# Kernel optimization log

Hardware: AMD Instinct MI355X
Metric: run time of the kernel (lower is better)

Reference implementation:

```python
import jax, jax.numpy as jnp
import numpy as np

N, E, H = 50000, 300000, 8  # nodes, edges, FeaStConv heads (PyG default)


def _lin_init(k, fan_in, fan_out):
    k1, k2 = jax.random.split(k)
    s = 1.0 / np.sqrt(fan_in)
    w = jax.random.uniform(k1, (fan_in, fan_out), jnp.float32, -s, s)
    b = jax.random.uniform(k2, (fan_out,), jnp.float32, -s, s)
    return w, b


def _conv_init(k, cin, cout):
    k1, k2 = jax.random.split(k)
    w = jax.random.normal(k1, (cin, H * cout), jnp.float32) * 0.1   # weight
    u = jax.random.normal(k2, (cin, H), jnp.float32) * 0.1          # attention u
    c = jnp.zeros((H,), jnp.float32)                                 # attention bias
    b = jnp.zeros((cout,), jnp.float32)                              # output bias
    return w, u, c, b


def setup_inputs() -> dict:
    key = jax.random.key(0)
    ks = jax.random.split(key, 10)
    x = jax.random.normal(ks[0], (N, 3), jnp.float32)
    src = jax.random.randint(ks[1], (E,), 0, N)
    dst = jax.random.randint(ks[2], (E,), 0, N)
    dst = jnp.where(src == dst, (dst + 1) % N, dst)  # no self loops in raw edge list
    edge_index = jnp.stack([src, dst]).astype(jnp.int64)
    labels = (jax.random.uniform(ks[3], (N, 1)) < 0.1).astype(jnp.float32)
    lin1_w, lin1_b = _lin_init(ks[4], 3, 16)
    c1_w, c1_u, c1_c, c1_b = _conv_init(ks[5], 16, 32)
    c2_w, c2_u, c2_c, c2_b = _conv_init(ks[6], 32, 64)
    c3_w, c3_u, c3_c, c3_b = _conv_init(ks[7], 64, 128)
    lin2_w, lin2_b = _lin_init(ks[8], 128, 1024)
    lin3_w, lin3_b = _lin_init(ks[9], 1024, 1)
    return dict(x=x, edge_index=edge_index, labels=labels,
                lin1_w=lin1_w, lin1_b=lin1_b,
                c1_w=c1_w, c1_u=c1_u, c1_c=c1_c, c1_b=c1_b,
                c2_w=c2_w, c2_u=c2_u, c2_c=c2_c, c2_b=c2_b,
                c3_w=c3_w, c3_u=c3_u, c3_c=c3_c, c3_b=c3_b,
                lin2_w=lin2_w, lin2_b=lin2_b, lin3_w=lin3_w, lin3_b=lin3_b)


def feast_conv(x, src, dst, W, u, c, b):
    """PyG FeaStConv: gather x_i/x_j, head-softmax attention on (x_j - x_i),
    per-edge weighted sum over heads, mean-scatter to destination nodes."""
    n = x.shape[0]
    loop = jnp.arange(n, dtype=src.dtype)
    s = jnp.concatenate([src, loop])  # add self loops (PyG default)
    d = jnp.concatenate([dst, loop])
    xi = x[d]
    xj = x[s]
    q = jax.nn.softmax((xj - xi) @ u + c, axis=-1)           # [E+N, H]
    m = (xj @ W).reshape(xj.shape[0], H, -1)                  # [E+N, H, O]
    msg = jnp.einsum('eh,eho->eo', q, m)                      # [E+N, O]
    agg = jax.ops.segment_sum(msg, d, num_segments=n)
    cnt = jax.ops.segment_sum(jnp.ones_like(d, dtype=msg.dtype), d, num_segments=n)
    return agg / cnt[:, None] + b                             # mean aggregation + bias


def reference(x, edge_index, labels,
              lin1_w, lin1_b,
              c1_w, c1_u, c1_c, c1_b,
              c2_w, c2_u, c2_c, c2_b,
              c3_w, c3_u, c3_c, c3_b,
              lin2_w, lin2_b, lin3_w, lin3_b):
    src, dst = edge_index[0], edge_index[1]
    h = jax.nn.relu(x @ lin1_w + lin1_b)
    h = jax.nn.relu(feast_conv(h, src, dst, c1_w, c1_u, c1_c, c1_b))
    h = jax.nn.relu(feast_conv(h, src, dst, c2_w, c2_u, c2_c, c2_b))
    h = jax.nn.relu(feast_conv(h, src, dst, c3_w, c3_u, c3_c, c3_b))
    h = jax.nn.relu(h @ lin2_w + lin2_b)
    p = jax.nn.sigmoid(h @ lin3_w + lin3_b)                   # [N, 1]
    # generate_weights: class-balanced per-element BCE weights
    n = labels.shape[0]
    pos = jnp.sum(labels)
    neg = n - pos
    w = jnp.where(labels == 1, n / (2.0 * pos), n / (2.0 * neg))
    # torch-style BCE with log clamped at -100
    bce = -(labels * jnp.clip(jnp.log(p), -100.0, None)
            + (1.0 - labels) * jnp.clip(jnp.log(1.0 - p), -100.0, None))
    loss = jnp.mean(w * bce)
    return loss, p
```

## Files before the change

### kernel.cpp

```cpp
#include <hip/hip_runtime.h>
#include <math.h>

#define NN 50000
#define NE 300000

typedef short s8v __attribute__((ext_vector_type(8)));
typedef float f4v __attribute__((ext_vector_type(4)));

__device__ inline unsigned short f2bf(float f) {
    union { float f; unsigned int u; } v; v.f = f;
    unsigned int r = v.u + 0x7FFFu + ((v.u >> 16) & 1u);
    return (unsigned short)(r >> 16);
}

__global__ void lin1_kernel(const float* __restrict__ x,
                            const float* __restrict__ w,
                            const float* __restrict__ b,
                            float* __restrict__ out) {
    int idx = blockIdx.x * 256 + threadIdx.x;
    if (idx >= NN * 16) return;
    int n = idx >> 4, o = idx & 15;
    float v = x[n*3+0]*w[o] + x[n*3+1]*w[16+o] + x[n*3+2]*w[32+o] + b[o];
    out[idx] = fmaxf(v, 0.f);
}

template<int CIN>
__global__ void a_kernel(const float* __restrict__ h,
                         const float* __restrict__ u,
                         float* __restrict__ a) {
    int idx = blockIdx.x * 256 + threadIdx.x;
    if (idx >= NN * 8) return;
    int n = idx >> 3, hd = idx & 7;
    float acc = 0.f;
    #pragma unroll
    for (int k = 0; k < CIN; ++k) acc += h[(size_t)n*CIN + k] * u[k*8 + hd];
    a[idx] = acc;
}

__global__ void hist_kernel(const int* __restrict__ dst, int* __restrict__ cnt) {
    int e = blockIdx.x * 256 + threadIdx.x;
    if (e < NE) atomicAdd(&cnt[dst[e]], 1);
}

__global__ void scan1_kernel(const int* __restrict__ cnt, int* __restrict__ rp,
                             int* __restrict__ bpart) {
    __shared__ int sh[256];
    int tid = threadIdx.x;
    int gid = blockIdx.x * 256 + tid;
    int v = (gid < NN) ? cnt[gid] : 0;
    sh[tid] = v;
    __syncthreads();
    for (int off = 1; off < 256; off <<= 1) {
        int t = (tid >= off) ? sh[tid - off] : 0;
        __syncthreads();
        sh[tid] += t;
        __syncthreads();
    }
    if (gid < NN) rp[gid] = sh[tid] - v;
    if (tid == 255) bpart[blockIdx.x] = sh[tid];
}

__global__ void scan2_kernel(int* __restrict__ bpart, int nblk) {
    __shared__ int sh[256];
    int tid = threadIdx.x;
    int v = (tid < nblk) ? bpart[tid] : 0;
    sh[tid] = v;
    __syncthreads();
    for (int off = 1; off < 256; off <<= 1) {
        int t = (tid >= off) ? sh[tid - off] : 0;
        __syncthreads();
        sh[tid] += t;
        __syncthreads();
    }
    bpart[tid] = sh[tid] - v;
}

__global__ void scan3_kernel(int* __restrict__ rp, const int* __restrict__ bpart) {
    int gid = blockIdx.x * 256 + threadIdx.x;
    if (gid < NN) rp[gid] += bpart[blockIdx.x];
    if (gid == 0) rp[NN] = NE;
}

__global__ void scatter_kernel(const int* __restrict__ src, const int* __restrict__ dst,
                               const int* __restrict__ rp, int* __restrict__ fill,
                               int* __restrict__ ssrc, int* __restrict__ sdst) {
    int e = blockIdx.x * 256 + threadIdx.x;
    if (e >= NE) return;
    int d = dst[e];
    int pos = rp[d] + atomicAdd(&fill[d], 1);
    ssrc[pos] = src[e];
    sdst[pos] = d;
}

__global__ void q_sorted_kernel(const int* __restrict__ ssrc,
                                const int* __restrict__ sdst,
                                const float* __restrict__ a,
                                const float* __restrict__ c,
                                float* __restrict__ qs) {
    int j = blockIdx.x * 256 + threadIdx.x;
    if (j >= NE) return;
    int s = ssrc[j], d = sdst[j];
    const float4* as = (const float4*)(a + (size_t)s*8);
    const float4* ad = (const float4*)(a + (size_t)d*8);
    float4 s0 = as[0], s1 = as[1], d0 = ad[0], d1 = ad[1];
    float lg[8] = { s0.x-d0.x+c[0], s0.y-d0.y+c[1], s0.z-d0.z+c[2], s0.w-d0.w+c[3],
                    s1.x-d1.x+c[4], s1.y-d1.y+c[5], s1.z-d1.z+c[6], s1.w-d1.w+c[7] };
    float m = lg[0];
    #pragma unroll
    for (int h = 1; h < 8; ++h) m = fmaxf(m, lg[h]);
    float sum = 0.f;
    #pragma unroll
    for (int h = 0; h < 8; ++h) { lg[h] = __expf(lg[h]-m); sum += lg[h]; }
    float inv = 1.f / sum;
    float4* qp = (float4*)(qs + (size_t)j*8);
    qp[0] = make_float4(lg[0]*inv, lg[1]*inv, lg[2]*inv, lg[3]*inv);
    qp[1] = make_float4(lg[4]*inv, lg[5]*inv, lg[6]*inv, lg[7]*inv);
}

template<int HPER>
__device__ inline void load_qv(const float* __restrict__ qs, int j, int hg, float* qv) {
    if constexpr (HPER == 2) {
        float2 t = *(const float2*)(qs + (size_t)j*8 + hg*2);
        qv[0] = t.x; qv[1] = t.y;
    } else if constexpr (HPER == 4) {
        float4 t = *(const float4*)(qs + (size_t)j*8 + hg*4);
        qv[0] = t.x; qv[1] = t.y; qv[2] = t.z; qv[3] = t.w;
    } else {
        float4 t0 = *(const float4*)(qs + (size_t)j*8);
        float4 t1 = *(const float4*)(qs + (size_t)j*8 + 4);
        qv[0] = t0.x; qv[1] = t0.y; qv[2] = t0.z; qv[3] = t0.w;
        qv[4] = t1.x; qv[5] = t1.y; qv[6] = t1.z; qv[7] = t1.w;
    }
}

template<int CIN>
__global__ __launch_bounds__(256) void agg_kernel(
        const float* __restrict__ hin, const float* __restrict__ cbias,
        const int* __restrict__ rowptr, const int* __restrict__ ssrc,
        const float* __restrict__ qs, unsigned short* __restrict__ g) {
    constexpr int HPER = CIN / 8;
    constexpr int LG = (CIN == 16) ? 4 : (CIN == 32) ? 5 : 6;
    const int lane = threadIdx.x & 63;
    const int d = blockIdx.x * 4 + (threadIdx.x >> 6);
    const int k = lane & (CIN - 1);
    const int hg = lane >> LG;
    float m = cbias[0];
    #pragma unroll
    for (int h = 1; h < 8; ++h) m = fmaxf(m, cbias[h]);
    float ssum = 0.f;
    #pragma unroll
    for (int h = 0; h < 8; ++h) ssum += __expf(cbias[h] - m);
    float sinv = 1.f / ssum;
    float xd = hin[(size_t)d*CIN + k];
    float acc[HPER];
    #pragma unroll
    for (int i = 0; i < HPER; ++i)
        acc[i] = __expf(cbias[hg*HPER + i] - m) * sinv * xd;
    int j0 = rowptr[d], j1 = rowptr[d+1];
    int j = j0;
    for (; j + 2 <= j1; j += 2) {
        int s0 = ssrc[j], s1 = ssrc[j+1];
        float xv0 = hin[(size_t)s0*CIN + k];
        float xv1 = hin[(size_t)s1*CIN + k];
        float qv0[HPER], qv1[HPER];
        load_qv<HPER>(qs, j, hg, qv0);
        load_qv<HPER>(qs, j+1, hg, qv1);
        #pragma unroll
        for (int i = 0; i < HPER; ++i) acc[i] += qv0[i]*xv0 + qv1[i]*xv1;
    }
    if (j < j1) {
        int s0 = ssrc[j];
        float xv0 = hin[(size_t)s0*CIN + k];
        float qv0[HPER];
        load_qv<HPER>(qs, j, hg, qv0);
        #pragma unroll
        for (int i = 0; i < HPER; ++i) acc[i] += qv0[i]*xv0;
    }
    #pragma unroll
    for (int i = 0; i < HPER; ++i)
        g[(size_t)d*(8*CIN) + (hg*HPER + i)*CIN + k] = f2bf(acc[i]);
}

template<int CIN, int O>
__global__ void packw_feast(const float* __restrict__ W, unsigned short* __restrict__ wp) {
    constexpr int NS = (8*CIN) / 32;
    constexpr int TOT = (O/16) * NS * 64;
    int t = blockIdx.x * 256 + threadIdx.x;
    if (t >= TOT) return;
    int l = t & 63;
    int s = (t >> 6) % NS;
    int ct = t / (64 * NS);
    int c = ct*16 + (l & 15);
    int kk0 = s*32 + (l >> 4) * 8;
    union { unsigned short u[8]; s8v v; } o;
    #pragma unroll
    for (int i = 0; i < 8; ++i) {
        int kk = kk0 + i;
        int h = kk / CIN, k = kk & (CIN - 1);
        o.u[i] = f2bf(W[(size_t)k*(8*O) + h*O + c]);
    }
    *(s8v*)(wp + (size_t)t*8) = o.v;
}

__global__ void packw_lin(const float* __restrict__ W, unsigned short* __restrict__ wp) {
    int t = blockIdx.x * 256 + threadIdx.x;
    if (t >= 64*4*64) return;
    int l = t & 63;
    int s = (t >> 6) & 3;
    int ctg = t >> 8;
    int c = ctg*16 + (l & 15);
    int k0 = s*32 + (l >> 4) * 8;
    union { unsigned short u[8]; s8v v; } o;
    #pragma unroll
    for (int i = 0; i < 8; ++i) o.u[i] = f2bf(W[(size_t)(k0+i)*1024 + c]);
    *(s8v*)(wp + (size_t)t*8) = o.v;
}

template<int K, int O, int CH, bool BF16OUT>
__global__ __launch_bounds__(256) void gemm_feast(
        const unsigned short* __restrict__ g, const unsigned short* __restrict__ wp,
        const int* __restrict__ rowptr, const float* __restrict__ b,
        float* __restrict__ houtf, unsigned short* __restrict__ houtb) {
    constexpr int NS = K / 32;
    constexpr int NCT = O / 16;
    __shared__ unsigned short bsh[CH*NS*64*8];
    const int l = threadIdx.x & 63;
    const int w = threadIdx.x >> 6;
    const int base = blockIdx.x * 64 + w * 16;
    int arow = base + (l & 15); if (arow >= NN) arow = NN - 1;
    const int koff = (l >> 4) * 8;
    s8v af[NS];
    #pragma unroll
    for (int s = 0; s < NS; ++s)
        af[s] = *(const s8v*)(g + (size_t)arow*K + s*32 + koff);
    float invc[4];
    #pragma unroll
    for (int r = 0; r < 4; ++r) {
        int n = base + (l >> 4)*4 + r; if (n >= NN) n = NN - 1;
        invc[r] = 1.f / (float)(rowptr[n+1] - rowptr[n] + 1);
    }
    #pragma unroll 1
    for (int ct0 = 0; ct0 < NCT; ct0 += CH) {
        __syncthreads();
        const int4* sp = (const int4*)(wp + (size_t)ct0*NS*512);
        int4* dp = (int4*)bsh;
        #pragma unroll 1
        for (int i = threadIdx.x; i < CH*NS*64; i += 256) dp[i] = sp[i];
        __syncthreads();
        #pragma unroll 1
        for (int cc = 0; cc < CH; ++cc) {
            f4v acc = {0.f, 0.f, 0.f, 0.f};
            #pragma unroll
            for (int s = 0; s < NS; ++s) {
                s8v bf = *(const s8v*)(bsh + ((size_t)(cc*NS + s)*64 + l)*8);
                acc = __builtin_amdgcn_mfma_f32_16x16x32_bf16(af[s], bf, acc, 0, 0, 0);
            }
            int col = (ct0 + cc)*16 + (l & 15);
            float bb = b[col];
            #pragma unroll
            for (int r = 0; r < 4; ++r) {
                int n = base + (l >> 4)*4 + r;
                float v = fmaxf(acc[r]*invc[r] + bb, 0.f);
                if (n < NN) {
                    if constexpr (BF16OUT) houtb[(size_t)n*O + col] = f2bf(v);
                    else                   houtf[(size_t)n*O + col] = v;
                }
            }
        }
    }
}

__global__ __launch_bounds__(256) void lin23_mfma(
        const unsigned short* __restrict__ h4b, const unsigned short* __restrict__ w2p,
        const float* __restrict__ b2, const float* __restrict__ w3,
        const float* __restrict__ b3, float* __restrict__ p) {
    constexpr int CH = 8;
    __shared__ unsigned short bsh[CH*4*64*8];
    const int l = threadIdx.x & 63;
    const int w = threadIdx.x >> 6;
    const int base = blockIdx.x * 64 + w * 16;
    int arow = base + (l & 15); if (arow >= NN) arow = NN - 1;
    const int koff = (l >> 4) * 8;
    s8v af[4];
    #pragma unroll
    for (int s = 0; s < 4; ++s)
        af[s] = *(const s8v*)(h4b + (size_t)arow*128 + s*32 + koff);
    float zp0 = 0.f, zp1 = 0.f, zp2 = 0.f, zp3 = 0.f;
    #pragma unroll 1
    for (int ct0 = 0; ct0 < 64; ct0 += CH) {
        __syncthreads();
        const int4* sp = (const int4*)(w2p + (size_t)ct0*4*512);
        int4* dp = (int4*)bsh;
        #pragma unroll 1
        for (int i = threadIdx.x; i < CH*4*64; i += 256) dp[i] = sp[i];
        __syncthreads();
        #pragma unroll 1
        for (int cc = 0; cc < CH; ++cc) {
            f4v acc = {0.f, 0.f, 0.f, 0.f};
            #pragma unroll
            for (int s = 0; s < 4; ++s) {
                s8v bf = *(const s8v*)(bsh + ((size_t)(cc*4 + s)*64 + l)*8);
                acc = __builtin_amdgcn_mfma_f32_16x16x32_bf16(af[s], bf, acc, 0, 0, 0);
            }
            int col = (ct0 + cc)*16 + (l & 15);
            float w3c = w3[col], bb = b2[col];
            zp0 += fmaxf(acc[0] + bb, 0.f) * w3c;
            zp1 += fmaxf(acc[1] + bb, 0.f) * w3c;
            zp2 += fmaxf(acc[2] + bb, 0.f) * w3c;
            zp3 += fmaxf(acc[3] + bb, 0.f) * w3c;
        }
    }
    #pragma unroll
    for (int off = 1; off < 16; off <<= 1) {
        zp0 += __shfl_xor(zp0, off, 64);
        zp1 += __shfl_xor(zp1, off, 64);
        zp2 += __shfl_xor(zp2, off, 64);
        zp3 += __shfl_xor(zp3, off, 64);
    }
    if ((l & 15) == 0) {
        int r0 = base + (l >> 4) * 4;
        float bb3 = b3[0];
        if (r0+0 < NN) p[r0+0] = 1.f / (1.f + expf(-(zp0 + bb3)));
        if (r0+1 < NN) p[r0+1] = 1.f / (1.f + expf(-(zp1 + bb3)));
        if (r0+2 < NN) p[r0+2] = 1.f / (1.f + expf(-(zp2 + bb3)));
        if (r0+3 < NN) p[r0+3] = 1.f / (1.f + expf(-(zp3 + bb3)));
    }
}

__global__ void loss_pass_kernel(const float* __restrict__ labels,
                                 const float* __restrict__ p,
                                 float* __restrict__ scal) {
    __shared__ float sh0[256], sh1[256], sh2[256];
    int tid = threadIdx.x;
    float pos = 0.f, sp = 0.f, sn = 0.f;
    for (int n = blockIdx.x*256 + tid; n < NN; n += gridDim.x*256) {
        float yv = labels[n], pv = p[n];
        if (yv == 1.0f) { pos += 1.f; sp -= fmaxf(logf(pv), -100.f); }
        else            { sn -= fmaxf(logf(1.f - pv), -100.f); }
    }
    sh0[tid] = pos; sh1[tid] = sp; sh2[tid] = sn;
    __syncthreads();
    for (int off = 128; off; off >>= 1) {
        if (tid < off) {
            sh0[tid] += sh0[tid+off];
            sh1[tid] += sh1[tid+off];
            sh2[tid] += sh2[tid+off];
        }
        __syncthreads();
    }
    if (tid == 0) {
        atomicAdd(&scal[0], sh0[0]);
        atomicAdd(&scal[1], sh1[0]);
        atomicAdd(&scal[2], sh2[0]);
    }
}

__global__ void loss_final_kernel(const float* __restrict__ scal,
                                  float* __restrict__ out) {
    float pos = scal[0];
    out[0] = scal[1] / (2.f*pos) + scal[2] / (2.f*((float)NN - pos));
}

extern "C" void kernel_launch(void* const* d_in, const int* in_sizes, int n_in,
                              void* d_out, int out_size, void* d_ws, size_t ws_size,
                              hipStream_t stream) {
    (void)in_sizes; (void)n_in; (void)out_size; (void)ws_size;
    const float* x   = (const float*)d_in[0];
    const int*   ei  = (const int*)d_in[1];
    const float* labels = (const float*)d_in[2];
    const float* l1w = (const float*)d_in[3];
    const float* l1b = (const float*)d_in[4];
    const float* cw[3] = {(const float*)d_in[5], (const float*)d_in[9],  (const float*)d_in[13]};
    const float* cu[3] = {(const float*)d_in[6], (const float*)d_in[10], (const float*)d_in[14]};
    const float* cc[3] = {(const float*)d_in[7], (const float*)d_in[11], (const float*)d_in[15]};
    const float* cb[3] = {(const float*)d_in[8], (const float*)d_in[12], (const float*)d_in[16]};
    const float* l2w = (const float*)d_in[17];
    const float* l2b = (const float*)d_in[18];
    const float* l3w = (const float*)d_in[19];
    const float* l3b = (const float*)d_in[20];
    const int* srcp = ei;
    const int* dstp = ei + NE;
    float* out = (float*)d_out;

    float* ws = (float*)d_ws;
    size_t off = 0;
    auto alloc = [&](size_t n) { float* p = ws + off; off += (n + 15) & ~(size_t)15; return p; };
    float* hA = alloc((size_t)NN*64);
    float* hB = alloc((size_t)NN*128);
    float* a  = alloc((size_t)NN*8);
    unsigned short* g  = (unsigned short*)alloc((size_t)NN*256);
    unsigned short* w2p = (unsigned short*)alloc(65536);
    unsigned short* wfp = (unsigned short*)alloc(32768);
    float* scal = alloc(16);
    int* rowptr = (int*)alloc(50016);
    int* fill   = (int*)alloc(50000);
    int* ssrc   = (int*)alloc(NE);
    int* sdst   = (int*)alloc(NE);
    int* bpart  = (int*)alloc(256);
    float* qs1 = hB;
    float* qs2 = hA;
    float* qs3 = hB;
    unsigned short* h4b = (unsigned short*)hB;

    const int SCAN_BLKS = (NN + 255) / 256;
    const int GB = (NN + 63) / 64;

    hipMemsetAsync(fill, 0, NN*sizeof(int), stream);
    hist_kernel<<<(NE+255)/256, 256, 0, stream>>>(dstp, fill);
    scan1_kernel<<<SCAN_BLKS, 256, 0, stream>>>(fill, rowptr, bpart);
    scan2_kernel<<<1, 256, 0, stream>>>(bpart, SCAN_BLKS);
    scan3_kernel<<<SCAN_BLKS, 256, 0, stream>>>(rowptr, bpart);
    hipMemsetAsync(fill, 0, NN*sizeof(int), stream);
    scatter_kernel<<<(NE+255)/256, 256, 0, stream>>>(srcp, dstp, rowptr, fill, ssrc, sdst);

    lin1_kernel<<<(NN*16+255)/256, 256, 0, stream>>>(x, l1w, l1b, hA);

    a_kernel<16><<<(NN*8+255)/256, 256, 0, stream>>>(hA, cu[0], a);
    q_sorted_kernel<<<(NE+255)/256, 256, 0, stream>>>(ssrc, sdst, a, cc[0], qs1);
    agg_kernel<16><<<NN/4, 256, 0, stream>>>(hA, cc[0], rowptr, ssrc, qs1, g);
    packw_feast<16,32><<<2, 256, 0, stream>>>(cw[0], wfp);
    gemm_feast<128,32,2,false><<<GB, 256, 0, stream>>>(g, wfp, rowptr, cb[0], hB, nullptr);

    a_kernel<32><<<(NN*8+255)/256, 256, 0, stream>>>(hB, cu[1], a);
    q_sorted_kernel<<<(NE+255)/256, 256, 0, stream>>>(ssrc, sdst, a, cc[1], qs2);
    agg_kernel<32><<<NN/4, 256, 0, stream>>>(hB, cc[1], rowptr, ssrc, qs2, g);
    packw_feast<32,64><<<8, 256, 0, stream>>>(cw[1], wfp);
    gemm_feast<256,64,4,false><<<GB, 256, 0, stream>>>(g, wfp, rowptr, cb[1], hA, nullptr);

    a_kernel<64><<<(NN*8+255)/256, 256, 0, stream>>>(hA, cu[2], a);
    q_sorted_kernel<<<(NE+255)/256, 256, 0, stream>>>(ssrc, sdst, a, cc[2], qs3);
    agg_kernel<64><<<NN/4, 256, 0, stream>>>(hA, cc[2], rowptr, ssrc, qs3, g);
    packw_feast<64,128><<<32, 256, 0, stream>>>(cw[2], wfp);
    gemm_feast<512,128,2,true><<<GB, 256, 0, stream>>>(g, wfp, rowptr, cb[2], nullptr, h4b);

    packw_lin<<<64, 256, 0, stream>>>(l2w, w2p);
    lin23_mfma<<<GB, 256, 0, stream>>>(h4b, w2p, l2b, l3w, l3b, out + 1);

    hipMemsetAsync(scal, 0, 16*sizeof(float), stream);
    loss_pass_kernel<<<256, 256, 0, stream>>>(labels, out + 1, scal);
    loss_final_kernel<<<1, 1, 0, stream>>>(scal, out);
}
```

Measured before the change: 283.1 us.

## Merge weight packing and memsets into one prep kernel; split lin2/lin3 across column groups

Weight packing for all layers and the buffer zeroing are folded into a single prep kernel launched at the start, which removes several small launches and memsets. The lin2/lin3 kernel is restructured so each block keeps a 64-column slice of the packed weights in registers and works over 256 rows. Partial logits are accumulated into z with atomics, and a separate sigmoid kernel produces p. The MFMA chains in the GEMM are split into two independent accumulators to shorten dependency chains, at the cost of float atomics and an extra launch.

```diff
diff --git a/kernel.cpp b/kernel.cpp
--- a/kernel.cpp
+++ b/kernel.cpp
@@ -182,11 +182,9 @@
 }
 
 template<int CIN, int O>
-__global__ void packw_feast(const float* __restrict__ W, unsigned short* __restrict__ wp) {
+__device__ inline void packw_feast_body(const float* __restrict__ W,
+                                        unsigned short* __restrict__ wp, int t) {
     constexpr int NS = (8*CIN) / 32;
-    constexpr int TOT = (O/16) * NS * 64;
-    int t = blockIdx.x * 256 + threadIdx.x;
-    if (t >= TOT) return;
     int l = t & 63;
     int s = (t >> 6) % NS;
     int ct = t / (64 * NS);
@@ -202,9 +200,8 @@
     *(s8v*)(wp + (size_t)t*8) = o.v;
 }
 
-__global__ void packw_lin(const float* __restrict__ W, unsigned short* __restrict__ wp) {
-    int t = blockIdx.x * 256 + threadIdx.x;
-    if (t >= 64*4*64) return;
+__device__ inline void packw_lin_body(const float* __restrict__ W,
+                                      unsigned short* __restrict__ wp, int t) {
     int l = t & 63;
     int s = (t >> 6) & 3;
     int ctg = t >> 8;
@@ -214,6 +211,29 @@
     #pragma unroll
     for (int i = 0; i < 8; ++i) o.u[i] = f2bf(W[(size_t)(k0+i)*1024 + c]);
     *(s8v*)(wp + (size_t)t*8) = o.v;
+}
+
+__global__ void prep_kernel(const float* __restrict__ l2w, unsigned short* __restrict__ w2p,
+                            const float* __restrict__ wf1w, unsigned short* __restrict__ wf1,
+                            const float* __restrict__ wf2w, unsigned short* __restrict__ wf2,
+                            const float* __restrict__ wf3w, unsigned short* __restrict__ wf3,
+                            int* __restrict__ fill, int* __restrict__ fill2,
+                            float* __restrict__ z, float* __restrict__ scal) {
+    int b = blockIdx.x;
+    int tid = threadIdx.x;
+    if (b < 64)  { packw_lin_body(l2w, w2p, b*256 + tid); return; }
+    b -= 64;
+    if (b < 2)   { packw_feast_body<16,32>(wf1w, wf1, b*256 + tid); return; }
+    b -= 2;
+    if (b < 8)   { packw_feast_body<32,64>(wf2w, wf2, b*256 + tid); return; }
+    b -= 8;
+    if (b < 32)  { packw_feast_body<64,128>(wf3w, wf3, b*256 + tid); return; }
+    b -= 32;
+    int idx = b*256 + tid;
+    if (idx < NN)            fill[idx] = 0;
+    else if (idx < 2*NN)     fill2[idx - NN] = 0;
+    else if (idx < 3*NN)     z[idx - 2*NN] = 0.f;
+    else if (idx < 3*NN+16)  scal[idx - 3*NN] = 0.f;
 }
 
 template<int K, int O, int CH, bool BF16OUT>
@@ -249,18 +269,23 @@
         __syncthreads();
         #pragma unroll 1
         for (int cc = 0; cc < CH; ++cc) {
-            f4v acc = {0.f, 0.f, 0.f, 0.f};
+            f4v accA = {0.f,0.f,0.f,0.f}, accB = {0.f,0.f,0.f,0.f};
             #pragma unroll
-            for (int s = 0; s < NS; ++s) {
+            for (int s = 0; s < NS/2; ++s) {
                 s8v bf = *(const s8v*)(bsh + ((size_t)(cc*NS + s)*64 + l)*8);
-                acc = __builtin_amdgcn_mfma_f32_16x16x32_bf16(af[s], bf, acc, 0, 0, 0);
+                accA = __builtin_amdgcn_mfma_f32_16x16x32_bf16(af[s], bf, accA, 0, 0, 0);
+            }
+            #pragma unroll
+            for (int s = NS/2; s < NS; ++s) {
+                s8v bf = *(const s8v*)(bsh + ((size_t)(cc*NS + s)*64 + l)*8);
+                accB = __builtin_amdgcn_mfma_f32_16x16x32_bf16(af[s], bf, accB, 0, 0, 0);
             }
             int col = (ct0 + cc)*16 + (l & 15);
             float bb = b[col];
             #pragma unroll
             for (int r = 0; r < 4; ++r) {
                 int n = base + (l >> 4)*4 + r;
-                float v = fmaxf(acc[r]*invc[r] + bb, 0.f);
+                float v = fmaxf((accA[r]+accB[r])*invc[r] + bb, 0.f);
                 if (n < NN) {
                     if constexpr (BF16OUT) houtb[(size_t)n*O + col] = f2bf(v);
                     else                   houtf[(size_t)n*O + col] = v;
@@ -270,61 +295,73 @@
     }
 }
 
-__global__ __launch_bounds__(256) void lin23_mfma(
+__global__ __launch_bounds__(256) void lin23z_kernel(
         const unsigned short* __restrict__ h4b, const unsigned short* __restrict__ w2p,
         const float* __restrict__ b2, const float* __restrict__ w3,
-        const float* __restrict__ b3, float* __restrict__ p) {
-    constexpr int CH = 8;
-    __shared__ unsigned short bsh[CH*4*64*8];
+        float* __restrict__ z) {
     const int l = threadIdx.x & 63;
     const int w = threadIdx.x >> 6;
-    const int base = blockIdx.x * 64 + w * 16;
-    int arow = base + (l & 15); if (arow >= NN) arow = NN - 1;
+    const int ctg = blockIdx.y;
+    const int rowbase = blockIdx.x * 256 + w * 64;
     const int koff = (l >> 4) * 8;
-    s8v af[4];
-    #pragma unroll
-    for (int s = 0; s < 4; ++s)
-        af[s] = *(const s8v*)(h4b + (size_t)arow*128 + s*32 + koff);
-    float zp0 = 0.f, zp1 = 0.f, zp2 = 0.f, zp3 = 0.f;
+    s8v bf0[4], bf1[4], bf2[4], bf3[4];
+    #pragma unroll
+    for (int s = 0; s < 4; ++s) {
+        bf0[s] = *(const s8v*)(w2p + ((size_t)((ctg*4+0)*4 + s)*64 + l)*8);
+        bf1[s] = *(const s8v*)(w2p + ((size_t)((ctg*4+1)*4 + s)*64 + l)*8);
+        bf2[s] = *(const s8v*)(w2p + ((size_t)((ctg*4+2)*4 + s)*64 + l)*8);
+        bf3[s] = *(const s8v*)(w2p + ((size_t)((ctg*4+3)*4 + s)*64 + l)*8);
+    }
+    float w3c[4], b2c[4];
+    #pragma unroll
+    for (int c = 0; c < 4; ++c) {
+        int col = (ctg*4 + c)*16 + (l & 15);
+        w3c[c] = w3[col]; b2c[c] = b2[col];
+    }
     #pragma unroll 1
-    for (int ct0 = 0; ct0 < 64; ct0 += CH) {
-        __syncthreads();
-        const int4* sp = (const int4*)(w2p + (size_t)ct0*4*512);
-        int4* dp = (int4*)bsh;
-        #pragma unroll 1
-        for (int i = threadIdx.x; i < CH*4*64; i += 256) dp[i] = sp[i];
-        __syncthreads();
-        #pragma unroll 1
-        for (int cc = 0; cc < CH; ++cc) {
-            f4v acc = {0.f, 0.f, 0.f, 0.f};
-            #pragma unroll
-            for (int s = 0; s < 4; ++s) {
-                s8v bf = *(const s8v*)(bsh + ((size_t)(cc*4 + s)*64 + l)*8);
-                acc = __builtin_amdgcn_mfma_f32_16x16x32_bf16(af[s], bf, acc, 0, 0, 0);
-            }
-            int col = (ct0 + cc)*16 + (l & 15);
-            float w3c = w3[col], bb = b2[col];
-            zp0 += fmaxf(acc[0] + bb, 0.f) * w3c;
-            zp1 += fmaxf(acc[1] + bb, 0.f) * w3c;
-            zp2 += fmaxf(acc[2] + bb, 0.f) * w3c;
-            zp3 += fmaxf(acc[3] + bb, 0.f) * w3c;
+    for (int t = 0; t < 4; ++t) {
+        int base = rowbase + t*16;
+        int arow = base + (l & 15); if (arow >= NN) arow = NN - 1;
+        s8v af[4];
+        #pragma unroll
+        for (int s = 0; s < 4; ++s)
+            af[s] = *(const s8v*)(h4b + (size_t)arow*128 + s*32 + koff);
+        float zp0 = 0.f, zp1 = 0.f, zp2 = 0.f, zp3 = 0.f;
+        #pragma unroll
+        for (int c = 0; c < 4; ++c) {
+            const s8v* bf = (c == 0) ? bf0 : (c == 1) ? bf1 : (c == 2) ? bf2 : bf3;
+            f4v accA = {0.f,0.f,0.f,0.f}, accB = {0.f,0.f,0.f,0.f};
+            accA = __builtin_amdgcn_mfma_f32_16x16x32_bf16(af[0], bf[0], accA, 0, 0, 0);
+            accA = __builtin_amdgcn_mfma_f32_16x16x32_bf16(af[1], bf[1], accA, 0, 0, 0);
+            accB = __builtin_amdgcn_mfma_f32_16x16x32_bf16(af[2], bf[2], accB, 0, 0, 0);
+            accB = __builtin_amdgcn_mfma_f32_16x16x32_bf16(af[3], bf[3], accB, 0, 0, 0);
+            zp0 += fmaxf(accA[0]+accB[0] + b2c[c], 0.f) * w3c[c];
+            zp1 += fmaxf(accA[1]+accB[1] + b2c[c], 0.f) * w3c[c];
+            zp2 += fmaxf(accA[2]+accB[2] + b2c[c], 0.f) * w3c[c];
+            zp3 += fmaxf(accA[3]+accB[3] + b2c[c], 0.f) * w3c[c];
         }
-    }
-    #pragma unroll
-    for (int off = 1; off < 16; off <<= 1) {
-        zp0 += __shfl_xor(zp0, off, 64);
-        zp1 += __shfl_xor(zp1, off, 64);
-        zp2 += __shfl_xor(zp2, off, 64);
-        zp3 += __shfl_xor(zp3, off, 64);
-    }
-    if ((l & 15) == 0) {
-        int r0 = base + (l >> 4) * 4;
-        float bb3 = b3[0];
-        if (r0+0 < NN) p[r0+0] = 1.f / (1.f + expf(-(zp0 + bb3)));
-        if (r0+1 < NN) p[r0+1] = 1.f / (1.f + expf(-(zp1 + bb3)));
-        if (r0+2 < NN) p[r0+2] = 1.f / (1.f + expf(-(zp2 + bb3)));
-        if (r0+3 < NN) p[r0+3] = 1.f / (1.f + expf(-(zp3 + bb3)));
-    }
+        #pragma unroll
+        for (int m = 1; m < 16; m <<= 1) {
+            zp0 += __shfl_xor(zp0, m, 64);
+            zp1 += __shfl_xor(zp1, m, 64);
+            zp2 += __shfl_xor(zp2, m, 64);
+            zp3 += __shfl_xor(zp3, m, 64);
+        }
+        if ((l & 15) == 0) {
+            int r0 = base + (l >> 4) * 4;
+            if (r0+0 < NN) atomicAdd(&z[r0+0], zp0);
+            if (r0+1 < NN) atomicAdd(&z[r0+1], zp1);
+            if (r0+2 < NN) atomicAdd(&z[r0+2], zp2);
+            if (r0+3 < NN) atomicAdd(&z[r0+3], zp3);
+        }
+    }
+}
+
+__global__ void sigmoid_kernel(const float* __restrict__ z,
+                               const float* __restrict__ b3,
+                               float* __restrict__ p) {
+    int n = blockIdx.x * 256 + threadIdx.x;
+    if (n < NN) p[n] = 1.f / (1.f + expf(-(z[n] + b3[0])));
 }
 
 __global__ void loss_pass_kernel(const float* __restrict__ labels,
@@ -388,12 +425,16 @@
     float* hA = alloc((size_t)NN*64);
     float* hB = alloc((size_t)NN*128);
     float* a  = alloc((size_t)NN*8);
-    unsigned short* g  = (unsigned short*)alloc((size_t)NN*256);
+    unsigned short* g   = (unsigned short*)alloc((size_t)NN*256);
     unsigned short* w2p = (unsigned short*)alloc(65536);
-    unsigned short* wfp = (unsigned short*)alloc(32768);
+    unsigned short* wf1 = (unsigned short*)alloc(2048);
+    unsigned short* wf2 = (unsigned short*)alloc(8192);
+    unsigned short* wf3 = (unsigned short*)alloc(32768);
+    float* z    = alloc(NN);
     float* scal = alloc(16);
     int* rowptr = (int*)alloc(50016);
-    int* fill   = (int*)alloc(50000);
+    int* fill   = (int*)alloc(NN);
+    int* fill2  = (int*)alloc(NN);
     int* ssrc   = (int*)alloc(NE);
     int* sdst   = (int*)alloc(NE);
     int* bpart  = (int*)alloc(256);
@@ -404,39 +445,36 @@
 
     const int SCAN_BLKS = (NN + 255) / 256;
     const int GB = (NN + 63) / 64;
-
-    hipMemsetAsync(fill, 0, NN*sizeof(int), stream);
+    const int PREP_BLKS = 106 + (3*NN + 16 + 255) / 256;
+
+    prep_kernel<<<PREP_BLKS, 256, 0, stream>>>(l2w, w2p, cw[0], wf1, cw[1], wf2,
+                                               cw[2], wf3, fill, fill2, z, scal);
     hist_kernel<<<(NE+255)/256, 256, 0, stream>>>(dstp, fill);
     scan1_kernel<<<SCAN_BLKS, 256, 0, stream>>>(fill, rowptr, bpart);
     scan2_kernel<<<1, 256, 0, stream>>>(bpart, SCAN_BLKS);
     scan3_kernel<<<SCAN_BLKS, 256, 0, stream>>>(rowptr, bpart);
-    hipMemsetAsync(fill, 0, NN*sizeof(int), stream);
-    scatter_kernel<<<(NE+255)/256, 256, 0, stream>>>(srcp, dstp, rowptr, fill, ssrc, sdst);
+    scatter_kernel<<<(NE+255)/256, 256, 0, stream>>>(srcp, dstp, rowptr, fill2, ssrc, sdst);
 
     lin1_kernel<<<(NN*16+255)/256, 256, 0, stream>>>(x, l1w, l1b, hA);
 
     a_kernel<16><<<(NN*8+255)/256, 256, 0, stream>>>(hA, cu[0], a);
     q_sorted_kernel<<<(NE+255)/256, 256, 0, stream>>>(ssrc, sdst, a, cc[0], qs1);
     agg_kernel<16><<<NN/4, 256, 0, stream>>>(hA, cc[0], rowptr, ssrc, qs1, g);
-    packw_feast<16,32><<<2, 256, 0, stream>>>(cw[0], wfp);
-    gemm_feast<128,32,2,false><<<GB, 256, 0, stream>>>(g, wfp, rowptr, cb[0], hB, nullptr);
+    gemm_feast<128,32,2,false><<<GB, 256, 0, stream>>>(g, wf1, rowptr, cb[0], hB, nullptr);
 
     a_kernel<32><<<(NN*8+255)/256, 256, 0, stream>>>(hB, cu[1], a);
     q_sorted_kernel<<<(NE+255)/256, 256, 0, stream>>>(ssrc, sdst, a, cc[1], qs2);
     agg_kernel<32><<<NN/4, 256, 0, stream>>>(hB, cc[1], rowptr, ssrc, qs2, g);
-    packw_feast<32,64><<<8, 256, 0, stream>>>(cw[1], wfp);
-    gemm_feast<256,64,4,false><<<GB, 256, 0, stream>>>(g, wfp, rowptr, cb[1], hA, nullptr);
+    gemm_feast<256,64,4,false><<<GB, 256, 0, stream>>>(g, wf2, rowptr, cb[1], hA, nullptr);
 
     a_kernel<64><<<(NN*8+255)/256, 256, 0, stream>>>(hA, cu[2], a);
     q_sorted_kernel<<<(NE+255)/256, 256, 0, stream>>>(ssrc, sdst, a, cc[2], qs3);
     agg_kernel<64><<<NN/4, 256, 0, stream>>>(hA, cc[2], rowptr, ssrc, qs3, g);
-    packw_feast<64,128><<<32, 256, 0, stream>>>(cw[2], wfp);
-    gemm_feast<512,128,2,true><<<GB, 256, 0, stream>>>(g, wfp, rowptr, cb[2], nullptr, h4b);
-
-    packw_lin<<<64, 256, 0, stream>>>(l2w, w2p);
-    lin23_mfma<<<GB, 256, 0, stream>>>(h4b, w2p, l2b, l3w, l3b, out + 1);
-
-    hipMemsetAsync(scal, 0, 16*sizeof(float), stream);
+    gemm_feast<512,128,2,true><<<GB, 256, 0, stream>>>(g, wf3, rowptr, cb[2], nullptr, h4b);
+
+    lin23z_kernel<<<dim3((NN+255)/256, 16), 256, 0, stream>>>(h4b, w2p, l2b, l3w, z);
+    sigmoid_kernel<<<SCAN_BLKS, 256, 0, stream>>>(z, l3b, out + 1);
+
     loss_pass_kernel<<<256, 256, 0, stream>>>(labels, out + 1, scal);
     loss_final_kernel<<<1, 1, 0, stream>>>(scal, out);
 }
```

After: 271.2 us. -4.2%, faster.
